# Kernel optimization log

Hardware: AMD Instinct MI355X
Metric: run time of the kernel (lower is better)

The kernel has to match this reference:

```python
import jax, jax.numpy as jnp
import numpy as np

D = 1024
H = 16
DK = D // H  # 64
CHUNK = 64
EPS = 1e-5


def setup_inputs() -> dict:
    key = jax.random.key(0)
    k1, k2, k3 = jax.random.split(key, 3)
    x = jax.random.normal(k1, (4, 4096, D), dtype=jnp.float32)
    W_qkv = jax.random.normal(k2, (D, 3 * D), dtype=jnp.float32) * 0.02
    W_o = jax.random.normal(k3, (D, D), dtype=jnp.float32) * 0.02
    return {"x": x, "W_qkv": W_qkv, "W_o": W_o}


def _layernorm_noaffine(k):
    mu = jnp.mean(k, axis=-1, keepdims=True)
    var = jnp.mean((k - mu) ** 2, axis=-1, keepdims=True)  # biased var, torch LayerNorm
    return (k - mu) / jnp.sqrt(var + EPS)


def _linear_attn(x, W_qkv, W_o):
    B, L, Dm = x.shape
    qkv = (x @ W_qkv).reshape(B, L, 3, H, DK)
    q, k, v = qkv[:, :, 0], qkv[:, :, 1], qkv[:, :, 2]
    k = _layernorm_noaffine(k)

    nC = L // CHUNK
    # [nC, B, C, H, DK] for scan over chunks
    to_chunks = lambda t: t.reshape(B, nC, CHUNK, H, DK).transpose(1, 0, 2, 3, 4)
    qc, kc, vc = to_chunks(q), to_chunks(k), to_chunks(v)

    causal = jnp.tril(jnp.ones((CHUNK, CHUNK), dtype=bool))  # s <= t inclusive

    def step(S, chunk):
        q_c, k_c, v_c = chunk  # each [B, C, H, DK]
        # inter-chunk: y_t += S_prev @ q_t
        inter = jnp.einsum('bhde,bthe->bthd', S, q_c)
        # intra-chunk: y_t += sum_{s<=t} (k_s . q_t) v_s
        scores = jnp.einsum('bthd,bshd->bhts', q_c, k_c)
        scores = jnp.where(causal, scores, 0.0)
        intra = jnp.einsum('bhts,bshd->bthd', scores, v_c)
        # state update: S += sum_t v_t k_t^T
        S = S + jnp.einsum('bthd,bthe->bhde', v_c, k_c)
        return S, inter + intra

    S0 = jnp.zeros((B, H, DK, DK), dtype=x.dtype)
    _, ys = jax.lax.scan(step, S0, (qc, kc, vc))  # ys: [nC, B, C, H, DK]
    y = ys.transpose(1, 0, 2, 3, 4).reshape(B, L, Dm)
    return y @ W_o


def reference(x, W_qkv, W_o):
    return _linear_attn(x, W_qkv, W_o)
```

## Files before the change

### kernel.cpp

```cpp
#include <hip/hip_runtime.h>

#define EPS 1e-5f

typedef __attribute__((ext_vector_type(8))) short s16x8;
typedef __attribute__((ext_vector_type(4))) float f4;

__device__ __forceinline__ short f2bf(float f) {
  union { float f; unsigned u; } x; x.f = f;
  unsigned r = x.u + 0x7fffu + ((x.u >> 16) & 1u);
  return (short)(r >> 16);
}
__device__ __forceinline__ float bf2f(short s) {
  union { unsigned u; float f; } x; x.u = ((unsigned)(unsigned short)s) << 16;
  return x.f;
}
__device__ __forceinline__ void gll16(const short* g, short* l) {
  __builtin_amdgcn_global_load_lds((const __attribute__((address_space(1))) void*)g,
                                   (__attribute__((address_space(3))) void*)l, 16, 0, 0);
}

__global__ __launch_bounds__(256) void cast_x(
    const float* __restrict__ x, short* __restrict__ xb)
{
  const size_t i = ((size_t)blockIdx.x * 256 + threadIdx.x) * 8;
  const float4* p = reinterpret_cast<const float4*>(x + i);
  float4 a = p[0], b = p[1];
  union { uint4 v; short s[8]; } o;
  o.s[0] = f2bf(a.x); o.s[1] = f2bf(a.y); o.s[2] = f2bf(a.z); o.s[3] = f2bf(a.w);
  o.s[4] = f2bf(b.x); o.s[5] = f2bf(b.y); o.s[6] = f2bf(b.z); o.s[7] = f2bf(b.w);
  *reinterpret_cast<uint4*>(xb + i) = o.v;
}

__global__ __launch_bounds__(256) void transpose_cast(
    const float* __restrict__ W, short* __restrict__ WT, int K, int N)
{
  __shared__ float tile[32][33];
  const int n0 = blockIdx.x * 32, k0 = blockIdx.y * 32;
  const int tx = threadIdx.x & 31, ty = threadIdx.x >> 5;
  #pragma unroll
  for (int i = 0; i < 4; i++) {
    int r = ty + i * 8;
    tile[r][tx] = W[(size_t)(k0 + r) * N + n0 + tx];
  }
  __syncthreads();
  #pragma unroll
  for (int i = 0; i < 4; i++) {
    int r = ty + i * 8;
    WT[(size_t)(n0 + r) * K + k0 + tx] = f2bf(tile[tx][r]);
  }
}

__global__ __launch_bounds__(256) void gemm_qkv_v3(
    const short* __restrict__ A, const short* __restrict__ BT,
    short* __restrict__ qb, short* __restrict__ kb, short* __restrict__ vb)
{
  __shared__ __align__(16) short lds[4 * 64 * 68];
  short* As = lds;
  short* Bs = lds + 4096;

  const int p = blockIdx.x;
  const int slot = p >> 3;
  const int strip = (p & 7) + 8 * (slot / 24);
  const int nb = slot % 24;
  const int m0 = strip * 128, n0 = nb * 128;

  const int tid = threadIdx.x;
  const int w = tid >> 6, lane = tid & 63, quad = lane >> 4, l16 = lane & 15;
  const int wm = (w >> 1) << 6, wn = (w & 1) << 6;

  f4 acc[4][4];
  #pragma unroll
  for (int i = 0; i < 4; i++)
    #pragma unroll
    for (int j = 0; j < 4; j++) acc[i][j] = {0.f, 0.f, 0.f, 0.f};

  const int row = w * 32 + (lane >> 2), ofs = (lane & 3) << 3;

  for (int k0 = 0; k0 < 1024; k0 += 32) {
    __syncthreads();
    gll16(A + (size_t)(m0 + row) * 1024 + k0 + ofs, &As[(w * 32) * 32]);
    gll16(A + (size_t)(m0 + row + 16) * 1024 + k0 + ofs, &As[(w * 32 + 16) * 32]);
    gll16(BT + (size_t)(n0 + row) * 1024 + k0 + ofs, &Bs[(w * 32) * 32]);
    gll16(BT + (size_t)(n0 + row + 16) * 1024 + k0 + ofs, &Bs[(w * 32 + 16) * 32]);
    __syncthreads();
    s16x8 afr[4], bfr[4];
    #pragma unroll
    for (int t = 0; t < 4; t++)
      afr[t] = *reinterpret_cast<const s16x8*>(&As[(wm + t * 16 + l16) * 32 + quad * 8]);
    #pragma unroll
    for (int t = 0; t < 4; t++)
      bfr[t] = *reinterpret_cast<const s16x8*>(&Bs[(wn + t * 16 + l16) * 32 + quad * 8]);
    #pragma unroll
    for (int ti = 0; ti < 4; ti++)
      #pragma unroll
      for (int tj = 0; tj < 4; tj++)
        acc[ti][tj] = __builtin_amdgcn_mfma_f32_16x16x32_bf16(afr[ti], bfr[tj], acc[ti][tj], 0, 0, 0);
  }

  __syncthreads();
  short* st = &lds[w * 64 * 68];
  #pragma unroll
  for (int ti = 0; ti < 4; ti++)
    #pragma unroll
    for (int tj = 0; tj < 4; tj++)
      #pragma unroll
      for (int r = 0; r < 4; r++)
        st[(ti * 16 + quad * 4 + r) * 68 + tj * 16 + l16] = f2bf(acc[ti][tj][r]);
  const int j0 = n0 + wn;
  const int sq = j0 >> 10;
  const int hh = (j0 >> 6) & 15;
  short* dbuf = (sq == 0) ? qb : (sq == 1) ? kb : vb;
  const int rr = lane >> 3, c8 = (lane & 7) << 3;
  #pragma unroll
  for (int it = 0; it < 8; it++) {
    int i = m0 + wm + it * 8 + rr;
    int bb = i >> 12, ll = i & 4095;
    uint4 val = *reinterpret_cast<const uint4*>(&st[(it * 8 + rr) * 68 + c8]);
    *reinterpret_cast<uint4*>(&dbuf[(((size_t)(bb * 16 + hh)) * 4096 + ll) * 64 + c8]) = val;
  }
}

__global__ __launch_bounds__(256) void ln_k(short* __restrict__ kbuf)
{
  const int row = blockIdx.x * 4 + (threadIdx.x >> 6);
  const int lane = threadIdx.x & 63;
  const size_t idx = (size_t)row * 64 + lane;
  float v = bf2f(kbuf[idx]);
  float s = v, s2 = v * v;
  #pragma unroll
  for (int off = 32; off; off >>= 1) {
    s += __shfl_xor(s, off);
    s2 += __shfl_xor(s2, off);
  }
  float mean = s * (1.f / 64.f);
  float var = s2 * (1.f / 64.f) - mean * mean;
  float rstd = rsqrtf(var + EPS);
  kbuf[idx] = f2bf((v - mean) * rstd);
}

__global__ __launch_bounds__(256) void chunk_outer(
    const short* __restrict__ kb, const short* __restrict__ vb,
    short* __restrict__ G)
{
  __shared__ __align__(16) short kT[64 * 72];
  __shared__ __align__(16) short vT[64 * 72];
  const int bh = blockIdx.x >> 6, c = blockIdx.x & 63;
  const int tid = threadIdx.x;
  const int w = tid >> 6, lane = tid & 63, quad = lane >> 4, l16 = lane & 15;
  const int srow = tid >> 2, sseg = (tid & 3) << 4;
  const size_t base = (size_t)bh * 262144 + (size_t)(c * 64 + srow) * 64 + sseg;

  {
    const float4* kp = reinterpret_cast<const float4*>(kb + base);
    union { float4 v[2]; short s[16]; } ku;
    ku.v[0] = kp[0]; ku.v[1] = kp[1];
    float kv[16]; float s = 0.f, s2 = 0.f;
    #pragma unroll
    for (int i = 0; i < 16; i++) { kv[i] = bf2f(ku.s[i]); s += kv[i]; s2 += kv[i] * kv[i]; }
    s += __shfl_xor(s, 1);  s2 += __shfl_xor(s2, 1);
    s += __shfl_xor(s, 2);  s2 += __shfl_xor(s2, 2);
    float mean = s * (1.f / 64.f);
    float var = s2 * (1.f / 64.f) - mean * mean;
    float rstd = rsqrtf(var + EPS);
    #pragma unroll
    for (int i = 0; i < 16; i++) kT[(sseg + i) * 72 + srow] = f2bf((kv[i] - mean) * rstd);
    const float4* vp = reinterpret_cast<const float4*>(vb + base);
    union { float4 v[2]; short s[16]; } vu;
    vu.v[0] = vp[0]; vu.v[1] = vp[1];
    #pragma unroll
    for (int i = 0; i < 16; i++) vT[(sseg + i) * 72 + srow] = vu.s[i];
  }
  __syncthreads();
  s16x8 va0 = *reinterpret_cast<const s16x8*>(&vT[(w * 16 + l16) * 72 + quad * 8]);
  s16x8 va1 = *reinterpret_cast<const s16x8*>(&vT[(w * 16 + l16) * 72 + 32 + quad * 8]);
  short* Gc = G + ((size_t)blockIdx.x) * 4096;
  #pragma unroll
  for (int tj = 0; tj < 4; tj++) {
    s16x8 kb0 = *reinterpret_cast<const s16x8*>(&kT[(tj * 16 + l16) * 72 + quad * 8]);
    s16x8 kb1 = *reinterpret_cast<const s16x8*>(&kT[(tj * 16 + l16) * 72 + 32 + quad * 8]);
    f4 z = {0.f, 0.f, 0.f, 0.f};
    z = __builtin_amdgcn_mfma_f32_16x16x32_bf16(va0, kb0, z, 0, 0, 0);
    z = __builtin_amdgcn_mfma_f32_16x16x32_bf16(va1, kb1, z, 0, 0, 0);
    #pragma unroll
    for (int r = 0; r < 4; r++)
      Gc[(w * 16 + quad * 4 + r) * 64 + tj * 16 + l16] = f2bf(z[r]);
  }
}

__global__ __launch_bounds__(256) void prefix_S(short* __restrict__ G)
{
  const int bh = blockIdx.x >> 2, rg = blockIdx.x & 3;
  const size_t base = (size_t)bh * 262144 + rg * 1024 + threadIdx.x * 4;
  float s0 = 0.f, s1 = 0.f, s2 = 0.f, s3 = 0.f;
  for (int c = 0; c < 64; c++) {
    short* p = G + base + (size_t)c * 4096;
    union { uint2 v; short s[4]; } gu;
    gu.v = *reinterpret_cast<const uint2*>(p);
    float g0 = bf2f(gu.s[0]), g1 = bf2f(gu.s[1]), g2 = bf2f(gu.s[2]), g3 = bf2f(gu.s[3]);
    union { uint2 v; short s[4]; } su;
    su.s[0] = f2bf(s0); su.s[1] = f2bf(s1); su.s[2] = f2bf(s2); su.s[3] = f2bf(s3);
    *reinterpret_cast<uint2*>(p) = su.v;
    s0 += g0; s1 += g1; s2 += g2; s3 += g3;
  }
}

__global__ __launch_bounds__(256) void chunk_out(
    const short* __restrict__ qb, const short* __restrict__ kb,
    const short* __restrict__ vb, const short* __restrict__ S,
    short* __restrict__ yb)
{
  __shared__ __align__(16) short vT[64 * 72];
  __shared__ __align__(16) short Ps[64 * 72];
  const int bh = blockIdx.x >> 6, c = blockIdx.x & 63;
  const int b = bh >> 4, h = bh & 15;
  const int tid = threadIdx.x;
  const int w = tid >> 6, lane = tid & 63, quad = lane >> 4, l16 = lane & 15;
  const int srow = tid >> 2, sseg = (tid & 3) << 4;
  const size_t base = (size_t)bh * 262144 + (size_t)c * 4096;

  {
    const float4* vp = reinterpret_cast<const float4*>(vb + base + (size_t)srow * 64 + sseg);
    union { float4 v[2]; short s[16]; } vu;
    vu.v[0] = vp[0]; vu.v[1] = vp[1];
    #pragma unroll
    for (int i = 0; i < 16; i++) vT[(sseg + i) * 72 + srow] = vu.s[i];
  }
  s16x8 qa[4][2], kf[2], sf[2];
  #pragma unroll
  for (int ti = 0; ti < 4; ti++)
    #pragma unroll
    for (int kh = 0; kh < 2; kh++)
      qa[ti][kh] = *reinterpret_cast<const s16x8*>(
          qb + base + (size_t)(ti * 16 + l16) * 64 + kh * 32 + quad * 8);
  #pragma unroll
  for (int kh = 0; kh < 2; kh++) {
    kf[kh] = *reinterpret_cast<const s16x8*>(
        kb + base + (size_t)(w * 16 + l16) * 64 + kh * 32 + quad * 8);
    sf[kh] = *reinterpret_cast<const s16x8*>(
        S + base + (size_t)(w * 16 + l16) * 64 + kh * 32 + quad * 8);
  }
  {
    float kv[16]; float s = 0.f, s2 = 0.f;
    #pragma unroll
    for (int kh = 0; kh < 2; kh++)
      #pragma unroll
      for (int i = 0; i < 8; i++) {
        float f = bf2f(kf[kh][i]); kv[kh * 8 + i] = f; s += f; s2 += f * f;
      }
    s += __shfl_xor(s, 16);  s2 += __shfl_xor(s2, 16);
    s += __shfl_xor(s, 32);  s2 += __shfl_xor(s2, 32);
    float mean = s * (1.f / 64.f);
    float var = s2 * (1.f / 64.f) - mean * mean;
    float rstd = rsqrtf(var + EPS);
    #pragma unroll
    for (int kh = 0; kh < 2; kh++)
      #pragma unroll
      for (int i = 0; i < 8; i++)
        kf[kh][i] = f2bf((kv[kh * 8 + i] - mean) * rstd);
  }
  __syncthreads();
  #pragma unroll
  for (int ti = 0; ti < 4; ti++) {
    f4 z = {0.f, 0.f, 0.f, 0.f};
    z = __builtin_amdgcn_mfma_f32_16x16x32_bf16(qa[ti][0], kf[0], z, 0, 0, 0);
    z = __builtin_amdgcn_mfma_f32_16x16x32_bf16(qa[ti][1], kf[1], z, 0, 0, 0);
    #pragma unroll
    for (int r = 0; r < 4; r++) {
      int t = ti * 16 + quad * 4 + r;
      int s = w * 16 + l16;
      Ps[t * 72 + s] = (s <= t) ? f2bf(z[r]) : (short)0;
    }
  }
  __syncthreads();
  s16x8 vf0 = *reinterpret_cast<const s16x8*>(&vT[(w * 16 + l16) * 72 + quad * 8]);
  s16x8 vf1 = *reinterpret_cast<const s16x8*>(&vT[(w * 16 + l16) * 72 + 32 + quad * 8]);
  #pragma unroll
  for (int ti = 0; ti < 4; ti++) {
    f4 z = {0.f, 0.f, 0.f, 0.f};
    s16x8 p0 = *reinterpret_cast<const s16x8*>(&Ps[(ti * 16 + l16) * 72 + quad * 8]);
    s16x8 p1 = *reinterpret_cast<const s16x8*>(&Ps[(ti * 16 + l16) * 72 + 32 + quad * 8]);
    z = __builtin_amdgcn_mfma_f32_16x16x32_bf16(p0, vf0, z, 0, 0, 0);
    z = __builtin_amdgcn_mfma_f32_16x16x32_bf16(p1, vf1, z, 0, 0, 0);
    z = __builtin_amdgcn_mfma_f32_16x16x32_bf16(qa[ti][0], sf[0], z, 0, 0, 0);
    z = __builtin_amdgcn_mfma_f32_16x16x32_bf16(qa[ti][1], sf[1], z, 0, 0, 0);
    #pragma unroll
    for (int r = 0; r < 4; r++) {
      int t = ti * 16 + quad * 4 + r;
      int d = w * 16 + l16;
      yb[(((size_t)b * 4096) + c * 64 + t) * 1024 + h * 64 + d] = f2bf(z[r]);
    }
  }
}

__global__ __launch_bounds__(256) void gemm_out_v3(
    const short* __restrict__ A, const short* __restrict__ BT, float* __restrict__ C)
{
  __shared__ __align__(16) short As[128 * 32];
  __shared__ __align__(16) short Bs[128 * 32];
  const int p = blockIdx.x;
  const int slot = p >> 3;
  const int strip = (p & 7) + 8 * (slot >> 3);
  const int nb = slot & 7;
  const int m0 = strip * 128, n0 = nb * 128;
  const int tid = threadIdx.x;
  const int w = tid >> 6, lane = tid & 63, quad = lane >> 4, l16 = lane & 15;
  const int wm = (w >> 1) << 6, wn = (w & 1) << 6;

  f4 acc[4][4];
  #pragma unroll
  for (int i = 0; i < 4; i++)
    #pragma unroll
    for (int j = 0; j < 4; j++) acc[i][j] = {0.f, 0.f, 0.f, 0.f};

  const int row = w * 32 + (lane >> 2), ofs = (lane & 3) << 3;

  for (int k0 = 0; k0 < 1024; k0 += 32) {
    __syncthreads();
    gll16(A + (size_t)(m0 + row) * 1024 + k0 + ofs, &As[(w * 32) * 32]);
    gll16(A + (size_t)(m0 + row + 16) * 1024 + k0 + ofs, &As[(w * 32 + 16) * 32]);
    gll16(BT + (size_t)(n0 + row) * 1024 + k0 + ofs, &Bs[(w * 32) * 32]);
    gll16(BT + (size_t)(n0 + row + 16) * 1024 + k0 + ofs, &Bs[(w * 32 + 16) * 32]);
    __syncthreads();
    s16x8 afr[4], bfr[4];
    #pragma unroll
    for (int t = 0; t < 4; t++)
      afr[t] = *reinterpret_cast<const s16x8*>(&As[(wm + t * 16 + l16) * 32 + quad * 8]);
    #pragma unroll
    for (int t = 0; t < 4; t++)
      bfr[t] = *reinterpret_cast<const s16x8*>(&Bs[(wn + t * 16 + l16) * 32 + quad * 8]);
    #pragma unroll
    for (int ti = 0; ti < 4; ti++)
      #pragma unroll
      for (int tj = 0; tj < 4; tj++)
        acc[ti][tj] = __builtin_amdgcn_mfma_f32_16x16x32_bf16(afr[ti], bfr[tj], acc[ti][tj], 0, 0, 0);
  }
  #pragma unroll
  for (int ti = 0; ti < 4; ti++)
    #pragma unroll
    for (int tj = 0; tj < 4; tj++)
      #pragma unroll
      for (int r = 0; r < 4; r++) {
        int i = m0 + wm + ti * 16 + quad * 4 + r;
        int j = n0 + wn + tj * 16 + l16;
        C[(size_t)i * 1024 + j] = acc[ti][tj][r];
      }
}

__global__ __launch_bounds__(256) void gemm_qkv_r1(
    const float* __restrict__ A, const float* __restrict__ B,
    short* __restrict__ qb, short* __restrict__ kb, short* __restrict__ vb)
{
  __shared__ __align__(16) short As[128 * 40];
  __shared__ __align__(16) short Bs[128 * 40];
  const int n0 = blockIdx.x * 128;
  const int m0 = blockIdx.y * 128;
  const int tid = threadIdx.x;
  const int w = tid >> 6, lane = tid & 63, quad = lane >> 4, l16 = lane & 15;
  const int wm = (w >> 1) << 6, wn = (w & 1) << 6;
  f4 acc[4][4];
  #pragma unroll
  for (int i = 0; i < 4; i++)
    #pragma unroll
    for (int j = 0; j < 4; j++) acc[i][j] = {0.f, 0.f, 0.f, 0.f};
  const int arow = tid >> 1, aseg = (tid & 1) << 4;
  const int brow = tid >> 3, bseg = (tid & 7) << 4;
  for (int k0 = 0; k0 < 1024; k0 += 32) {
    __syncthreads();
    {
      const float4* ap = reinterpret_cast<const float4*>(A + (size_t)(m0 + arow) * 1024 + k0 + aseg);
      union { float4 v[4]; float f[16]; } af;
      af.v[0] = ap[0]; af.v[1] = ap[1]; af.v[2] = ap[2]; af.v[3] = ap[3];
      union { float4 v[2]; short s[16]; } ao;
      #pragma unroll
      for (int i = 0; i < 16; i++) ao.s[i] = f2bf(af.f[i]);
      float4* dst = reinterpret_cast<float4*>(&As[arow * 40 + aseg]);
      dst[0] = ao.v[0]; dst[1] = ao.v[1];
    }
    {
      const float4* bp = reinterpret_cast<const float4*>(B + (size_t)(k0 + brow) * 3072 + n0 + bseg);
      union { float4 v[4]; float f[16]; } bu;
      bu.v[0] = bp[0]; bu.v[1] = bp[1]; bu.v[2] = bp[2]; bu.v[3] = bp[3];
      #pragma unroll
      for (int i = 0; i < 16; i++) Bs[(bseg + i) * 40 + brow] = f2bf(bu.f[i]);
    }
    __syncthreads();
    s16x8 afr[4], bfr[4];
    #pragma unroll
    for (int t = 0; t < 4; t++)
      afr[t] = *reinterpret_cast<const s16x8*>(&As[(wm + t * 16 + l16) * 40 + quad * 8]);
    #pragma unroll
    for (int t = 0; t < 4; t++)
      bfr[t] = *reinterpret_cast<const s16x8*>(&Bs[(wn + t * 16 + l16) * 40 + quad * 8]);
    #pragma unroll
    for (int ti = 0; ti < 4; ti++)
      #pragma unroll
      for (int tj = 0; tj < 4; tj++)
        acc[ti][tj] = __builtin_amdgcn_mfma_f32_16x16x32_bf16(afr[ti], bfr[tj], acc[ti][tj], 0, 0, 0);
  }
  const int sq = n0 >> 10;
  short* dbuf = (sq == 0) ? qb : (sq == 1) ? kb : vb;
  #pragma unroll
  for (int ti = 0; ti < 4; ti++)
    #pragma unroll
    for (int tj = 0; tj < 4; tj++)
      #pragma unroll
      for (int r = 0; r < 4; r++) {
        int i = m0 + wm + ti * 16 + quad * 4 + r;
        int j = n0 + wn + tj * 16 + l16;
        int hh = (j >> 6) & 15, dd = j & 63;
        int bb = i >> 12, ll = i & 4095;
        dbuf[(((size_t)(bb * 16 + hh)) * 4096 + ll) * 64 + dd] = f2bf(acc[ti][tj][r]);
      }
}

__global__ __launch_bounds__(256) void scan_chunks_r1(
    const short* __restrict__ qb, const short* __restrict__ kb,
    const short* __restrict__ vb, short* __restrict__ yb)
{
  __shared__ __align__(16) short qs[64 * 72];
  __shared__ __align__(16) short ks[64 * 72];
  __shared__ __align__(16) short kT[64 * 72];
  __shared__ __align__(16) short vT[64 * 72];
  __shared__ __align__(16) short Sb[64 * 72];
  __shared__ __align__(16) short Ps[64 * 72];
  const int bh = blockIdx.x;
  const int b = bh >> 4, h = bh & 15;
  const int tid = threadIdx.x;
  const int w = tid >> 6, lane = tid & 63, quad = lane >> 4, l16 = lane & 15;
  const int srow = tid >> 2, sseg = (tid & 3) << 4;
  const size_t base = (size_t)bh * 4096 * 64;
  f4 accS[4];
  #pragma unroll
  for (int i = 0; i < 4; i++) accS[i] = {0.f, 0.f, 0.f, 0.f};
  for (int c = 0; c < 64; c++) {
    __syncthreads();
    {
      size_t g = base + ((size_t)(c * 64 + srow)) * 64 + sseg;
      const float4* qp = reinterpret_cast<const float4*>(qb + g);
      float4 q0 = qp[0], q1 = qp[1];
      *reinterpret_cast<float4*>(&qs[srow * 72 + sseg]) = q0;
      *reinterpret_cast<float4*>(&qs[srow * 72 + sseg + 8]) = q1;
      const float4* kp = reinterpret_cast<const float4*>(kb + g);
      union { float4 v[2]; short s[16]; } ku;
      ku.v[0] = kp[0]; ku.v[1] = kp[1];
      *reinterpret_cast<float4*>(&ks[srow * 72 + sseg]) = ku.v[0];
      *reinterpret_cast<float4*>(&ks[srow * 72 + sseg + 8]) = ku.v[1];
      #pragma unroll
      for (int i = 0; i < 16; i++) kT[(sseg + i) * 72 + srow] = ku.s[i];
      const float4* vp = reinterpret_cast<const float4*>(vb + g);
      union { float4 v[2]; short s[16]; } vu;
      vu.v[0] = vp[0]; vu.v[1] = vp[1];
      #pragma unroll
      for (int i = 0; i < 16; i++) vT[(sseg + i) * 72 + srow] = vu.s[i];
    }
    #pragma unroll
    for (int ti = 0; ti < 4; ti++)
      #pragma unroll
      for (int r = 0; r < 4; r++)
        Sb[(ti * 16 + quad * 4 + r) * 72 + w * 16 + l16] = f2bf(accS[ti][r]);
    __syncthreads();
    s16x8 qa[4][2];
    #pragma unroll
    for (int ti = 0; ti < 4; ti++)
      #pragma unroll
      for (int kh = 0; kh < 2; kh++)
        qa[ti][kh] = *reinterpret_cast<const s16x8*>(&qs[(ti * 16 + l16) * 72 + kh * 32 + quad * 8]);
    s16x8 kf[2];
    #pragma unroll
    for (int kh = 0; kh < 2; kh++)
      kf[kh] = *reinterpret_cast<const s16x8*>(&ks[(w * 16 + l16) * 72 + kh * 32 + quad * 8]);
    #pragma unroll
    for (int ti = 0; ti < 4; ti++) {
      f4 z = {0.f, 0.f, 0.f, 0.f};
      z = __builtin_amdgcn_mfma_f32_16x16x32_bf16(qa[ti][0], kf[0], z, 0, 0, 0);
      z = __builtin_amdgcn_mfma_f32_16x16x32_bf16(qa[ti][1], kf[1], z, 0, 0, 0);
      #pragma unroll
      for (int r = 0; r < 4; r++) {
        int t = ti * 16 + quad * 4 + r;
        int s = w * 16 + l16;
        Ps[t * 72 + s] = (s <= t) ? f2bf(z[r]) : (short)0;
      }
    }
    __syncthreads();
    s16x8 vf[2], sf[2];
    #pragma unroll
    for (int kh = 0; kh < 2; kh++) {
      vf[kh] = *reinterpret_cast<const s16x8*>(&vT[(w * 16 + l16) * 72 + kh * 32 + quad * 8]);
      sf[kh] = *reinterpret_cast<const s16x8*>(&Sb[(w * 16 + l16) * 72 + kh * 32 + quad * 8]);
    }
    #pragma unroll
    for (int ti = 0; ti < 4; ti++) {
      f4 z = {0.f, 0.f, 0.f, 0.f};
      s16x8 p0 = *reinterpret_cast<const s16x8*>(&Ps[(ti * 16 + l16) * 72 + quad * 8]);
      s16x8 p1 = *reinterpret_cast<const s16x8*>(&Ps[(ti * 16 + l16) * 72 + 32 + quad * 8]);
      z = __builtin_amdgcn_mfma_f32_16x16x32_bf16(p0, vf[0], z, 0, 0, 0);
      z = __builtin_amdgcn_mfma_f32_16x16x32_bf16(p1, vf[1], z, 0, 0, 0);
      z = __builtin_amdgcn_mfma_f32_16x16x32_bf16(qa[ti][0], sf[0], z, 0, 0, 0);
      z = __builtin_amdgcn_mfma_f32_16x16x32_bf16(qa[ti][1], sf[1], z, 0, 0, 0);
      #pragma unroll
      for (int r = 0; r < 4; r++) {
        int t = ti * 16 + quad * 4 + r;
        int d = w * 16 + l16;
        yb[(((size_t)b * 4096) + c * 64 + t) * 1024 + h * 64 + d] = f2bf(z[r]);
      }
    }
    s16x8 ku0 = *reinterpret_cast<const s16x8*>(&kT[(w * 16 + l16) * 72 + quad * 8]);
    s16x8 ku1 = *reinterpret_cast<const s16x8*>(&kT[(w * 16 + l16) * 72 + 32 + quad * 8]);
    #pragma unroll
    for (int ti = 0; ti < 4; ti++) {
      s16x8 va0 = *reinterpret_cast<const s16x8*>(&vT[(ti * 16 + l16) * 72 + quad * 8]);
      s16x8 va1 = *reinterpret_cast<const s16x8*>(&vT[(ti * 16 + l16) * 72 + 32 + quad * 8]);
      accS[ti] = __builtin_amdgcn_mfma_f32_16x16x32_bf16(va0, ku0, accS[ti], 0, 0, 0);
      accS[ti] = __builtin_amdgcn_mfma_f32_16x16x32_bf16(va1, ku1, accS[ti], 0, 0, 0);
    }
  }
}

__global__ __launch_bounds__(256) void gemm_out_r1(
    const short* __restrict__ A, const float* __restrict__ B, float* __restrict__ C)
{
  __shared__ __align__(16) short As[128 * 40];
  __shared__ __align__(16) short Bs[128 * 40];
  const int n0 = blockIdx.x * 128;
  const int m0 = blockIdx.y * 128;
  const int tid = threadIdx.x;
  const int w = tid >> 6, lane = tid & 63, quad = lane >> 4, l16 = lane & 15;
  const int wm = (w >> 1) << 6, wn = (w & 1) << 6;
  f4 acc[4][4];
  #pragma unroll
  for (int i = 0; i < 4; i++)
    #pragma unroll
    for (int j = 0; j < 4; j++) acc[i][j] = {0.f, 0.f, 0.f, 0.f};
  const int arow = tid >> 1, aseg = (tid & 1) << 4;
  const int brow = tid >> 3, bseg = (tid & 7) << 4;
  for (int k0 = 0; k0 < 1024; k0 += 32) {
    __syncthreads();
    {
      const float4* ap = reinterpret_cast<const float4*>(A + (size_t)(m0 + arow) * 1024 + k0 + aseg);
      float4 a0 = ap[0], a1 = ap[1];
      float4* dst = reinterpret_cast<float4*>(&As[arow * 40 + aseg]);
      dst[0] = a0; dst[1] = a1;
    }
    {
      const float4* bp = reinterpret_cast<const float4*>(B + (size_t)(k0 + brow) * 1024 + n0 + bseg);
      union { float4 v[4]; float f[16]; } bu;
      bu.v[0] = bp[0]; bu.v[1] = bp[1]; bu.v[2] = bp[2]; bu.v[3] = bp[3];
      #pragma unroll
      for (int i = 0; i < 16; i++) Bs[(bseg + i) * 40 + brow] = f2bf(bu.f[i]);
    }
    __syncthreads();
    s16x8 afr[4], bfr[4];
    #pragma unroll
    for (int t = 0; t < 4; t++)
      afr[t] = *reinterpret_cast<const s16x8*>(&As[(wm + t * 16 + l16) * 40 + quad * 8]);
    #pragma unroll
    for (int t = 0; t < 4; t++)
      bfr[t] = *reinterpret_cast<const s16x8*>(&Bs[(wn + t * 16 + l16) * 40 + quad * 8]);
    #pragma unroll
    for (int ti = 0; ti < 4; ti++)
      #pragma unroll
      for (int tj = 0; tj < 4; tj++)
        acc[ti][tj] = __builtin_amdgcn_mfma_f32_16x16x32_bf16(afr[ti], bfr[tj], acc[ti][tj], 0, 0, 0);
  }
  #pragma unroll
  for (int ti = 0; ti < 4; ti++)
    #pragma unroll
    for (int tj = 0; tj < 4; tj++)
      #pragma unroll
      for (int r = 0; r < 4; r++) {
        int i = m0 + wm + ti * 16 + quad * 4 + r;
        int j = n0 + wn + tj * 16 + l16;
        C[(size_t)i * 1024 + j] = acc[ti][tj][r];
      }
}

extern "C" void kernel_launch(void* const* d_in, const int* in_sizes, int n_in,
                              void* d_out, int out_size, void* d_ws, size_t ws_size,
                              hipStream_t stream) {
  const float* x    = (const float*)d_in[0];
  const float* Wqkv = (const float*)d_in[1];
  const float* Wo   = (const float*)d_in[2];
  float* out = (float*)d_out;

  short* qb = (short*)d_ws;
  short* kb = qb + (size_t)16777216;
  short* vb = kb + (size_t)16777216;
  short* yb = vb + (size_t)16777216;

  const size_t NEED = 176160768;
  if (ws_size >= NEED) {
    short* Gs    = yb + (size_t)16777216;
    short* WqkvT = Gs + (size_t)16777216;
    short* WoT   = WqkvT + (size_t)3145728;
    short* xb    = Gs;

    cast_x        <<<dim3(8192),    256, 0, stream>>>(x, xb);
    transpose_cast<<<dim3(96, 32),  256, 0, stream>>>(Wqkv, WqkvT, 1024, 3072);
    transpose_cast<<<dim3(32, 32),  256, 0, stream>>>(Wo, WoT, 1024, 1024);
    gemm_qkv_v3   <<<dim3(3072),    256, 0, stream>>>(xb, WqkvT, qb, kb, vb);
    chunk_outer   <<<dim3(4096),    256, 0, stream>>>(kb, vb, Gs);
    prefix_S      <<<dim3(256),     256, 0, stream>>>(Gs);
    chunk_out     <<<dim3(4096),    256, 0, stream>>>(qb, kb, vb, Gs, yb);
    gemm_out_v3   <<<dim3(1024),    256, 0, stream>>>(yb, WoT, out);
  } else {
    gemm_qkv_r1   <<<dim3(24, 128), 256, 0, stream>>>(x, Wqkv, qb, kb, vb);
    ln_k          <<<dim3(65536),   256, 0, stream>>>(kb);
    scan_chunks_r1<<<dim3(64),      256, 0, stream>>>(qb, kb, vb, yb);
    gemm_out_r1   <<<dim3(8, 128),  256, 0, stream>>>(yb, Wo, out);
  }
}
```

Baseline: 364.4 us.

## Merge prep kernels, shrink QKV GEMM epilogue LDS, split prefix scan finer

Folds the x cast and both weight transpose-casts into one launch, which removes two kernel launches. The QKV GEMM epilogue now stages one 16-row slice per wave at a time, cutting its LDS from about 34 KB to 16 KB so more blocks can share a CU. The prefix-sum kernel uses 512 blocks of 128 threads instead of 256 of 256, giving the serial 64-step scan more parallel blocks. The trade-off is extra barrier-free LDS round trips in the epilogue and some branch divergence in the merged prep kernel.

```diff
diff --git a/kernel.cpp b/kernel.cpp
--- a/kernel.cpp
+++ b/kernel.cpp
@@ -19,23 +19,28 @@
                                    (__attribute__((address_space(3))) void*)l, 16, 0, 0);
 }
 
-__global__ __launch_bounds__(256) void cast_x(
-    const float* __restrict__ x, short* __restrict__ xb)
-{
-  const size_t i = ((size_t)blockIdx.x * 256 + threadIdx.x) * 8;
-  const float4* p = reinterpret_cast<const float4*>(x + i);
-  float4 a = p[0], b = p[1];
-  union { uint4 v; short s[8]; } o;
-  o.s[0] = f2bf(a.x); o.s[1] = f2bf(a.y); o.s[2] = f2bf(a.z); o.s[3] = f2bf(a.w);
-  o.s[4] = f2bf(b.x); o.s[5] = f2bf(b.y); o.s[6] = f2bf(b.z); o.s[7] = f2bf(b.w);
-  *reinterpret_cast<uint4*>(xb + i) = o.v;
-}
-
-__global__ __launch_bounds__(256) void transpose_cast(
-    const float* __restrict__ W, short* __restrict__ WT, int K, int N)
+__global__ __launch_bounds__(256) void prep(
+    const float* __restrict__ x, const float* __restrict__ Wqkv,
+    const float* __restrict__ Wo,
+    short* __restrict__ xb, short* __restrict__ WqkvT, short* __restrict__ WoT)
 {
   __shared__ float tile[32][33];
-  const int n0 = blockIdx.x * 32, k0 = blockIdx.y * 32;
+  const int bid = blockIdx.x;
+  if (bid < 8192) {
+    const size_t i = ((size_t)bid * 256 + threadIdx.x) * 8;
+    const float4* p = reinterpret_cast<const float4*>(x + i);
+    float4 a = p[0], b = p[1];
+    union { uint4 v; short s[8]; } o;
+    o.s[0] = f2bf(a.x); o.s[1] = f2bf(a.y); o.s[2] = f2bf(a.z); o.s[3] = f2bf(a.w);
+    o.s[4] = f2bf(b.x); o.s[5] = f2bf(b.y); o.s[6] = f2bf(b.z); o.s[7] = f2bf(b.w);
+    *reinterpret_cast<uint4*>(xb + i) = o.v;
+    return;
+  }
+  const float* W; short* WT; int K, N, t;
+  if (bid < 11264) { W = Wqkv; WT = WqkvT; K = 1024; N = 3072; t = bid - 8192;  }
+  else             { W = Wo;   WT = WoT;   K = 1024; N = 1024; t = bid - 11264; }
+  const int nblk = N >> 5;
+  const int n0 = (t % nblk) * 32, k0 = (t / nblk) * 32;
   const int tx = threadIdx.x & 31, ty = threadIdx.x >> 5;
   #pragma unroll
   for (int i = 0; i < 4; i++) {
@@ -50,11 +55,11 @@
   }
 }
 
-__global__ __launch_bounds__(256) void gemm_qkv_v3(
+__global__ __launch_bounds__(256) void gemm_qkv_v4(
     const short* __restrict__ A, const short* __restrict__ BT,
     short* __restrict__ qb, short* __restrict__ kb, short* __restrict__ vb)
 {
-  __shared__ __align__(16) short lds[4 * 64 * 68];
+  __shared__ __align__(16) short lds[8192];
   short* As = lds;
   short* Bs = lds + 4096;
 
@@ -98,25 +103,27 @@
   }
 
   __syncthreads();
-  short* st = &lds[w * 64 * 68];
-  #pragma unroll
-  for (int ti = 0; ti < 4; ti++)
-    #pragma unroll
-    for (int tj = 0; tj < 4; tj++)
-      #pragma unroll
-      for (int r = 0; r < 4; r++)
-        st[(ti * 16 + quad * 4 + r) * 68 + tj * 16 + l16] = f2bf(acc[ti][tj][r]);
+  short* st = &lds[w * 16 * 72];
   const int j0 = n0 + wn;
   const int sq = j0 >> 10;
   const int hh = (j0 >> 6) & 15;
   short* dbuf = (sq == 0) ? qb : (sq == 1) ? kb : vb;
-  const int rr = lane >> 3, c8 = (lane & 7) << 3;
-  #pragma unroll
-  for (int it = 0; it < 8; it++) {
-    int i = m0 + wm + it * 8 + rr;
-    int bb = i >> 12, ll = i & 4095;
-    uint4 val = *reinterpret_cast<const uint4*>(&st[(it * 8 + rr) * 68 + c8]);
-    *reinterpret_cast<uint4*>(&dbuf[(((size_t)(bb * 16 + hh)) * 4096 + ll) * 64 + c8]) = val;
+  const int r2 = lane >> 3, c8 = (lane & 7) << 3;
+  #pragma unroll
+  for (int ti = 0; ti < 4; ti++) {
+    #pragma unroll
+    for (int tj = 0; tj < 4; tj++)
+      #pragma unroll
+      for (int r = 0; r < 4; r++)
+        st[(quad * 4 + r) * 72 + tj * 16 + l16] = f2bf(acc[ti][tj][r]);
+    #pragma unroll
+    for (int h2 = 0; h2 < 2; h2++) {
+      int rr = h2 * 8 + r2;
+      int i = m0 + wm + ti * 16 + rr;
+      int bb = i >> 12, ll = i & 4095;
+      uint4 val = *reinterpret_cast<const uint4*>(&st[rr * 72 + c8]);
+      *reinterpret_cast<uint4*>(&dbuf[(((size_t)(bb * 16 + hh)) * 4096 + ll) * 64 + c8]) = val;
+    }
   }
 }
 
@@ -187,10 +194,10 @@
   }
 }
 
-__global__ __launch_bounds__(256) void prefix_S(short* __restrict__ G)
-{
-  const int bh = blockIdx.x >> 2, rg = blockIdx.x & 3;
-  const size_t base = (size_t)bh * 262144 + rg * 1024 + threadIdx.x * 4;
+__global__ __launch_bounds__(128) void prefix_S(short* __restrict__ G)
+{
+  const int bh = blockIdx.x >> 3, rg = blockIdx.x & 7;
+  const size_t base = (size_t)bh * 262144 + rg * 512 + threadIdx.x * 4;
   float s0 = 0.f, s1 = 0.f, s2 = 0.f, s3 = 0.f;
   for (int c = 0; c < 64; c++) {
     short* p = G + base + (size_t)c * 4096;
@@ -594,12 +601,10 @@
     short* WoT   = WqkvT + (size_t)3145728;
     short* xb    = Gs;
 
-    cast_x        <<<dim3(8192),    256, 0, stream>>>(x, xb);
-    transpose_cast<<<dim3(96, 32),  256, 0, stream>>>(Wqkv, WqkvT, 1024, 3072);
-    transpose_cast<<<dim3(32, 32),  256, 0, stream>>>(Wo, WoT, 1024, 1024);
-    gemm_qkv_v3   <<<dim3(3072),    256, 0, stream>>>(xb, WqkvT, qb, kb, vb);
+    prep          <<<dim3(12288),   256, 0, stream>>>(x, Wqkv, Wo, xb, WqkvT, WoT);
+    gemm_qkv_v4   <<<dim3(3072),    256, 0, stream>>>(xb, WqkvT, qb, kb, vb);
     chunk_outer   <<<dim3(4096),    256, 0, stream>>>(kb, vb, Gs);
-    prefix_S      <<<dim3(256),     256, 0, stream>>>(Gs);
+    prefix_S      <<<dim3(512),     128, 0, stream>>>(Gs);
     chunk_out     <<<dim3(4096),    256, 0, stream>>>(qb, kb, vb, Gs, yb);
     gemm_out_v3   <<<dim3(1024),    256, 0, stream>>>(yb, WoT, out);
   } else {
```

New measurement: 356.6 us. -2.2%, faster.
